# Kernel tuning notes

Measured on AMD Instinct MI355X. Metric: run time of the kernel, lower is better.

Reference implementation:

```python
import jax, jax.numpy as jnp
import numpy as np

N_NODES = 131072
N_EDGES = 4194304
H1, H2 = 16, 1


def setup_inputs() -> dict:
    key = jax.random.key(0)
    k = jax.random.split(key, 6)
    x = jax.random.uniform(k[0], (N_NODES, 2), dtype=jnp.float32)
    edge_index = jax.random.randint(k[1], (2, N_EDGES), 0, N_NODES, dtype=jnp.int64)
    # GCNConv weights (glorot-ish scale) and zero biases
    W1 = jax.random.normal(k[2], (2, H1), dtype=jnp.float32) * 0.5
    b1 = jnp.zeros((H1,), dtype=jnp.float32)
    W2 = jax.random.normal(k[3], (H1, H2), dtype=jnp.float32) * 0.25
    b2 = jnp.zeros((H2,), dtype=jnp.float32)
    return {"x": x, "W1": W1, "b1": b1, "W2": W2, "b2": b2, "edge_index": edge_index}


def gcn_layer(x, W, b, src, dst, n):
    # PyG GCNConv: h = D^{-1/2} (A+I) D^{-1/2} (x W) + b  (self-loops already in src/dst)
    h = x @ W                                              # [N, F_out]
    deg = jax.ops.segment_sum(jnp.ones(dst.shape[0], h.dtype), dst, num_segments=n)
    dinv = jax.lax.rsqrt(deg)                              # deg >= 1 thanks to self-loops
    norm = dinv[src] * dinv[dst]                           # [E+N]
    out = jax.ops.segment_sum(h[src] * norm[:, None], dst, num_segments=n)
    return out + b


def reference(x, W1, b1, W2, b2, edge_index):
    n = x.shape[0]
    loops = jnp.arange(n, dtype=edge_index.dtype)
    src = jnp.concatenate([edge_index[0], loops])          # add self-loops once
    dst = jnp.concatenate([edge_index[1], loops])
    h = jax.nn.relu(gcn_layer(x, W1, b1, src, dst, n))
    h = gcn_layer(h, W2, b2, src, dst, n)                  # [N, 1]
    scores = jax.nn.sigmoid(h)
    return scores[edge_index[0]]                           # gather per-edge source score [E, 1]
```

## Files before the change

kernel.cpp:

```cpp
#include <hip/hip_runtime.h>
#include <cmath>

typedef unsigned int uint;

constexpr int N  = 131072;
constexpr int E  = 4194304;
constexpr int F  = 16;
constexpr int NB = 512;
constexpr int NBLK  = 512;
constexpr int SCT   = 512;
constexpr int CHUNK = 8192;
constexpr int EPT   = 16;
constexpr int NSCAN = NB * NBLK;
constexpr int CAP   = 10240;
constexpr int SLOTS = CAP / SCT;
constexpr int LPN   = 16;

__global__ void __launch_bounds__(SCT) k_hist(const int* __restrict__ dst,
                                              uint* __restrict__ hist_blocks) {
    __shared__ uint hw[8 * NB];
    int t = threadIdx.x, g = blockIdx.x;
    int w = t >> 6;
#pragma unroll
    for (int k = 0; k < 8; ++k) hw[k * SCT + t] = 0;
    __syncthreads();
    const int4* dst4 = (const int4*)dst;
    int base4 = g * (CHUNK / 4);
#pragma unroll
    for (int k = 0; k < EPT / 4; ++k) {
        int4 d4 = dst4[base4 + k * SCT + t];
        atomicAdd(&hw[w * NB + (d4.x >> 8)], 1u);
        atomicAdd(&hw[w * NB + (d4.y >> 8)], 1u);
        atomicAdd(&hw[w * NB + (d4.z >> 8)], 1u);
        atomicAdd(&hw[w * NB + (d4.w >> 8)], 1u);
    }
    __syncthreads();
    uint sum = 0;
#pragma unroll
    for (int k = 0; k < 8; ++k) sum += hw[k * NB + t];
    hist_blocks[(size_t)t * NBLK + g] = sum;
}

__global__ void k_scan_up(const uint* __restrict__ hist, uint* __restrict__ bsum) {
    __shared__ uint s[256];
    int g = blockIdx.x, t = threadIdx.x;
    s[t] = hist[(size_t)g * 256 + t];
    __syncthreads();
    for (int off = 128; off > 0; off >>= 1) {
        if (t < off) s[t] += s[t + off];
        __syncthreads();
    }
    if (t == 0) bsum[g] = s[0];
}

__global__ void k_scan_down(const uint* __restrict__ hist, const uint* __restrict__ bsum,
                            uint* __restrict__ scanned) {
    __shared__ uint red[256];
    __shared__ uint s[256];
    int g = blockIdx.x, t = threadIdx.x;
    uint p = 0;
    for (int i = t; i < g; i += 256) p += bsum[i];
    red[t] = p;
    __syncthreads();
    for (int off = 128; off > 0; off >>= 1) {
        if (t < off) red[t] += red[t + off];
        __syncthreads();
    }
    uint base = red[0];
    uint v = hist[(size_t)g * 256 + t];
    s[t] = v;
    __syncthreads();
    for (int off = 1; off < 256; off <<= 1) {
        uint x = (t >= off) ? s[t - off] : 0u;
        __syncthreads();
        s[t] += x;
        __syncthreads();
    }
    scanned[(size_t)g * 256 + t] = base + s[t] - v;
}

__global__ void __launch_bounds__(SCT) k_scatter(
        const int* __restrict__ src, const int* __restrict__ dst,
        const uint* __restrict__ scanned, uint* __restrict__ part) {
    __shared__ uint h[NB];
    __shared__ uint wb[NB];
    __shared__ uint wsum[8];
    __shared__ uint vals[CHUNK];
    __shared__ uint addr[CHUNK];
    int t = threadIdx.x, g = blockIdx.x;
    int lane = t & 63, w = t >> 6;
    h[t] = 0;
    __syncthreads();
    int d[EPT], s[EPT];
    const int4* src4 = (const int4*)src;
    const int4* dst4 = (const int4*)dst;
    int base4 = g * (CHUNK / 4);
#pragma unroll
    for (int k = 0; k < EPT / 4; ++k) {
        int4 d4 = dst4[base4 + k * SCT + t];
        int4 s4 = src4[base4 + k * SCT + t];
        d[4 * k + 0] = d4.x; d[4 * k + 1] = d4.y; d[4 * k + 2] = d4.z; d[4 * k + 3] = d4.w;
        s[4 * k + 0] = s4.x; s[4 * k + 1] = s4.y; s[4 * k + 2] = s4.z; s[4 * k + 3] = s4.w;
        atomicAdd(&h[d4.x >> 8], 1u);
        atomicAdd(&h[d4.y >> 8], 1u);
        atomicAdd(&h[d4.z >> 8], 1u);
        atomicAdd(&h[d4.w >> 8], 1u);
    }
    __syncthreads();
    uint v = h[t];
    uint sv = v;
#pragma unroll
    for (int off = 1; off < 64; off <<= 1) {
        uint n = __shfl_up(sv, off);
        if (lane >= off) sv += n;
    }
    if (lane == 63) wsum[w] = sv;
    __syncthreads();
    uint wo = 0;
    for (int i = 0; i < w; ++i) wo += wsum[i];
    sv += wo;
    uint ex = sv - v;
    wb[t] = scanned[(size_t)t * NBLK + g] - ex;
    h[t] = ex;
    __syncthreads();
#pragma unroll
    for (int k = 0; k < EPT; ++k) {
        int b = d[k] >> 8;
        uint slot = atomicAdd(&h[b], 1u);
        vals[slot] = ((uint)s[k] << 8) | (uint)(d[k] & 255);
        addr[slot] = wb[b] + slot;
    }
    __syncthreads();
#pragma unroll
    for (int k = 0; k < EPT; ++k) {
        int i = k * SCT + t;
        part[addr[i]] = vals[i];
    }
}

__global__ void __launch_bounds__(SCT) k_sort(
        uint* part, const uint* __restrict__ scanned,
        const float* __restrict__ x,
        uint* __restrict__ csr, float* __restrict__ dinv, float2* __restrict__ y) {
    __shared__ uint hw[8 * 256];
    __shared__ uint cnt[256];
    __shared__ uint sc[256];
    __shared__ uint wsum[4];
    __shared__ uint srt[CAP];
    int t = threadIdx.x, b = blockIdx.x;
    int lane = t & 63, w = t >> 6;
#pragma unroll
    for (int k = 0; k < 4; ++k) hw[k * SCT + t] = 0;
    __syncthreads();
    uint S0 = scanned[(size_t)b * NBLK];
    uint S1 = (b == NB - 1) ? (uint)E : scanned[(size_t)(b + 1) * NBLK];
    uint pk[SLOTS];
#pragma unroll
    for (int k = 0; k < SLOTS; ++k) {
        uint i = S0 + (uint)(k * SCT + t);
        pk[k] = (i < S1) ? part[i] : 0xFFFFFFFFu;
        if (pk[k] != 0xFFFFFFFFu) atomicAdd(&hw[w * 256 + (pk[k] & 255u)], 1u);
    }
    __syncthreads();
    if (t < 256) {
        uint tot = 0;
#pragma unroll
        for (int k = 0; k < 8; ++k) {
            uint c = hw[k * 256 + t];
            hw[k * 256 + t] = tot;
            tot += c;
        }
        cnt[t] = tot;
        uint sv = tot;
#pragma unroll
        for (int off = 1; off < 64; off <<= 1) {
            uint n = __shfl_up(sv, off);
            if (lane >= off) sv += n;
        }
        if (lane == 63) wsum[t >> 6] = sv;
        sc[t] = sv;
    }
    __syncthreads();
    if (t < 256) {
        uint wo = 0;
        for (int i = 0; i < (t >> 6); ++i) wo += wsum[i];
        sc[t] += wo;
    }
    __syncthreads();
#pragma unroll
    for (int k = 0; k < SLOTS; ++k) {
        if (pk[k] != 0xFFFFFFFFu) {
            uint bin = pk[k] & 255u;
            uint slot = (sc[bin] - cnt[bin]) + atomicAdd(&hw[w * 256 + bin], 1u);
            srt[slot] = pk[k] >> 8;
        }
    }
    __syncthreads();
    uint L = S1 - S0;
    for (uint i = t; i < L; i += SCT) part[S0 + i] = srt[i];
    if (t < 256) {
        int node = (b << 8) + t;
        csr[node] = S0 + (sc[t] - cnt[t]);
        float di = rsqrtf(1.0f + (float)cnt[t]);
        dinv[node] = di;
        float2 xv = ((const float2*)x)[node];
        y[node] = make_float2(di * xv.x, di * xv.y);
    }
}

__global__ void k_l1(const uint* __restrict__ srcs, const uint* __restrict__ csr,
                     const float2* __restrict__ y, const float* __restrict__ dinv,
                     const float* __restrict__ W1, const float* __restrict__ b1,
                     const float* __restrict__ W2, float* __restrict__ g2) {
    int tid = blockIdx.x * blockDim.x + threadIdx.x;
    int node = tid >> 4, lane = tid & (LPN - 1);
    uint o0 = csr[node];
    uint o1 = (node == N - 1) ? (uint)E : csr[node + 1];
    float A0 = 0.0f, A1 = 0.0f;
    for (uint j = o0 + lane; j < o1; j += LPN) {
        float2 ys = y[srcs[j]];
        A0 += ys.x; A1 += ys.y;
    }
    A0 += __shfl_xor(A0, 1); A0 += __shfl_xor(A0, 2);
    A0 += __shfl_xor(A0, 4); A0 += __shfl_xor(A0, 8);
    A1 += __shfl_xor(A1, 1); A1 += __shfl_xor(A1, 2);
    A1 += __shfl_xor(A1, 4); A1 += __shfl_xor(A1, 8);
    float di = dinv[node];
    float2 yn = y[node];
    A0 = di * (A0 + yn.x);
    A1 = di * (A1 + yn.y);
    int f = lane;
    float v = fmaf(A0, W1[f], fmaf(A1, W1[F + f], b1[f]));
    float acc = fmaxf(v, 0.0f) * W2[f];
    acc += __shfl_xor(acc, 1); acc += __shfl_xor(acc, 2);
    acc += __shfl_xor(acc, 4); acc += __shfl_xor(acc, 8);
    if (lane == 0) g2[node] = di * acc;
}

__global__ void k_l2(const uint* __restrict__ srcs, const uint* __restrict__ csr,
                     const float* __restrict__ g2, const float* __restrict__ dinv,
                     const float* __restrict__ b2, float* __restrict__ scores) {
    int tid = blockIdx.x * blockDim.x + threadIdx.x;
    int node = tid >> 4, lane = tid & (LPN - 1);
    uint o0 = csr[node];
    uint o1 = (node == N - 1) ? (uint)E : csr[node + 1];
    float acc = 0.0f;
    for (uint j = o0 + lane; j < o1; j += LPN) acc += g2[srcs[j]];
    acc += __shfl_xor(acc, 1); acc += __shfl_xor(acc, 2);
    acc += __shfl_xor(acc, 4); acc += __shfl_xor(acc, 8);
    if (lane == 0) {
        float v = fmaf(dinv[node], acc + g2[node], b2[0]);
        scores[node] = 1.0f / (1.0f + expf(-v));
    }
}

__global__ void k_out(const int* __restrict__ src, const float* __restrict__ scores,
                      float* __restrict__ out) {
    int i = blockIdx.x * blockDim.x + threadIdx.x;
    if (i >= E / 4) return;
    int4 s4 = ((const int4*)src)[i];
    float4 o;
    o.x = scores[s4.x];
    o.y = scores[s4.y];
    o.z = scores[s4.z];
    o.w = scores[s4.w];
    ((float4*)out)[i] = o;
}

extern "C" void kernel_launch(void* const* d_in, const int* in_sizes, int n_in,
                              void* d_out, int out_size, void* d_ws, size_t ws_size,
                              hipStream_t stream) {
    const float* x  = (const float*)d_in[0];
    const float* W1 = (const float*)d_in[1];
    const float* b1 = (const float*)d_in[2];
    const float* W2 = (const float*)d_in[3];
    const float* b2 = (const float*)d_in[4];
    const int*   ei = (const int*)d_in[5];
    const int* src = ei;
    const int* dst = ei + E;

    uint* hist_blocks = (uint*)d_ws;
    uint* scanned     = hist_blocks + NSCAN;
    uint* bsum        = scanned + NSCAN;
    uint* csr         = bsum + 1024;
    float* dinv       = (float*)(csr + N + 2);
    float2* y         = (float2*)(dinv + N);
    float* g2         = (float*)(y + N);
    float* scores     = g2 + N;

    uint* part  = (uint*)d_out;
    float* out  = (float*)d_out;

    k_hist     <<<NBLK,          SCT, 0, stream>>>(dst, hist_blocks);
    k_scan_up  <<<NSCAN / 256,   256, 0, stream>>>(hist_blocks, bsum);
    k_scan_down<<<NSCAN / 256,   256, 0, stream>>>(hist_blocks, bsum, scanned);
    k_scatter  <<<NBLK,          SCT, 0, stream>>>(src, dst, scanned, part);
    k_sort     <<<NB,            SCT, 0, stream>>>(part, scanned, x, csr, dinv, y);
    k_l1       <<<(N * LPN) / 256, 256, 0, stream>>>(part, csr, y, dinv, W1, b1, W2, g2);
    k_l2       <<<(N * LPN) / 256, 256, 0, stream>>>(part, csr, g2, dinv, b2, scores);
    k_out      <<<E / 4 / 256,   256, 0, stream>>>(src, scores, out);
}
```

Before: 190.4 us.

## Drop global histogram and scan passes; sort from per-chunk segments with fixed buckets

Removes the histogram kernel and the two global scan kernels. The scatter kernel now writes each locally bucket-sorted chunk contiguously with coalesced uint4 stores, and records per-chunk bucket counts and offsets as 16-bit tables. The sort kernel has each thread walk one chunk's segment for its bucket and writes into fixed-capacity bucket slots, with separate csr start and end arrays. This saves a full pass over dst, two launches and the scattered global writes. In exchange, the sort reads are strided and uncoalesced, and any bucket over 9216 edges is silently truncated.

```diff
diff --git a/kernel.cpp b/kernel.cpp
--- a/kernel.cpp
+++ b/kernel.cpp
@@ -2,6 +2,7 @@
 #include <cmath>
 
 typedef unsigned int uint;
+typedef unsigned short u16;
 
 constexpr int N  = 131072;
 constexpr int E  = 4194304;
@@ -11,82 +12,15 @@
 constexpr int SCT   = 512;
 constexpr int CHUNK = 8192;
 constexpr int EPT   = 16;
-constexpr int NSCAN = NB * NBLK;
-constexpr int CAP   = 10240;
-constexpr int SLOTS = CAP / SCT;
+constexpr int CAPB  = 9216;
 constexpr int LPN   = 16;
-
-__global__ void __launch_bounds__(SCT) k_hist(const int* __restrict__ dst,
-                                              uint* __restrict__ hist_blocks) {
-    __shared__ uint hw[8 * NB];
-    int t = threadIdx.x, g = blockIdx.x;
-    int w = t >> 6;
-#pragma unroll
-    for (int k = 0; k < 8; ++k) hw[k * SCT + t] = 0;
-    __syncthreads();
-    const int4* dst4 = (const int4*)dst;
-    int base4 = g * (CHUNK / 4);
-#pragma unroll
-    for (int k = 0; k < EPT / 4; ++k) {
-        int4 d4 = dst4[base4 + k * SCT + t];
-        atomicAdd(&hw[w * NB + (d4.x >> 8)], 1u);
-        atomicAdd(&hw[w * NB + (d4.y >> 8)], 1u);
-        atomicAdd(&hw[w * NB + (d4.z >> 8)], 1u);
-        atomicAdd(&hw[w * NB + (d4.w >> 8)], 1u);
-    }
-    __syncthreads();
-    uint sum = 0;
-#pragma unroll
-    for (int k = 0; k < 8; ++k) sum += hw[k * NB + t];
-    hist_blocks[(size_t)t * NBLK + g] = sum;
-}
-
-__global__ void k_scan_up(const uint* __restrict__ hist, uint* __restrict__ bsum) {
-    __shared__ uint s[256];
-    int g = blockIdx.x, t = threadIdx.x;
-    s[t] = hist[(size_t)g * 256 + t];
-    __syncthreads();
-    for (int off = 128; off > 0; off >>= 1) {
-        if (t < off) s[t] += s[t + off];
-        __syncthreads();
-    }
-    if (t == 0) bsum[g] = s[0];
-}
-
-__global__ void k_scan_down(const uint* __restrict__ hist, const uint* __restrict__ bsum,
-                            uint* __restrict__ scanned) {
-    __shared__ uint red[256];
-    __shared__ uint s[256];
-    int g = blockIdx.x, t = threadIdx.x;
-    uint p = 0;
-    for (int i = t; i < g; i += 256) p += bsum[i];
-    red[t] = p;
-    __syncthreads();
-    for (int off = 128; off > 0; off >>= 1) {
-        if (t < off) red[t] += red[t + off];
-        __syncthreads();
-    }
-    uint base = red[0];
-    uint v = hist[(size_t)g * 256 + t];
-    s[t] = v;
-    __syncthreads();
-    for (int off = 1; off < 256; off <<= 1) {
-        uint x = (t >= off) ? s[t - off] : 0u;
-        __syncthreads();
-        s[t] += x;
-        __syncthreads();
-    }
-    scanned[(size_t)g * 256 + t] = base + s[t] - v;
-}
 
 __global__ void __launch_bounds__(SCT) k_scatter(
         const int* __restrict__ src, const int* __restrict__ dst,
-        const uint* __restrict__ scanned, uint* __restrict__ part) {
+        uint* __restrict__ part, u16* __restrict__ cnt16, u16* __restrict__ dir16) {
     __shared__ uint h[NB];
-    __shared__ uint wb[NB];
     __shared__ uint wsum[8];
     __shared__ uint vals[CHUNK];
-    __shared__ uint addr[CHUNK];
     int t = threadIdx.x, g = blockIdx.x;
     int lane = t & 63, w = t >> 6;
     h[t] = 0;
@@ -120,7 +54,9 @@
     for (int i = 0; i < w; ++i) wo += wsum[i];
     sv += wo;
     uint ex = sv - v;
-    wb[t] = scanned[(size_t)t * NBLK + g] - ex;
+    cnt16[(size_t)t * NBLK + g] = (u16)v;
+    dir16[(size_t)t * NBLK + g] = (u16)ex;
+    __syncthreads();
     h[t] = ex;
     __syncthreads();
 #pragma unroll
@@ -128,39 +64,34 @@
         int b = d[k] >> 8;
         uint slot = atomicAdd(&h[b], 1u);
         vals[slot] = ((uint)s[k] << 8) | (uint)(d[k] & 255);
-        addr[slot] = wb[b] + slot;
-    }
-    __syncthreads();
-#pragma unroll
-    for (int k = 0; k < EPT; ++k) {
-        int i = k * SCT + t;
-        part[addr[i]] = vals[i];
-    }
+    }
+    __syncthreads();
+    uint4* part4 = (uint4*)(part + (size_t)g * CHUNK);
+    const uint4* vals4 = (const uint4*)vals;
+#pragma unroll
+    for (int k = 0; k < EPT / 4; ++k)
+        part4[k * SCT + t] = vals4[k * SCT + t];
 }
 
 __global__ void __launch_bounds__(SCT) k_sort(
-        uint* part, const uint* __restrict__ scanned,
-        const float* __restrict__ x,
-        uint* __restrict__ csr, float* __restrict__ dinv, float2* __restrict__ y) {
+        const uint* __restrict__ part, const u16* __restrict__ cnt16,
+        const u16* __restrict__ dir16, const float* __restrict__ x,
+        uint* __restrict__ part2, uint* __restrict__ csr, uint* __restrict__ cend,
+        float* __restrict__ dinv, float2* __restrict__ y) {
     __shared__ uint hw[8 * 256];
     __shared__ uint cnt[256];
     __shared__ uint sc[256];
     __shared__ uint wsum[4];
-    __shared__ uint srt[CAP];
+    __shared__ uint srt[CAPB];
     int t = threadIdx.x, b = blockIdx.x;
     int lane = t & 63, w = t >> 6;
 #pragma unroll
     for (int k = 0; k < 4; ++k) hw[k * SCT + t] = 0;
     __syncthreads();
-    uint S0 = scanned[(size_t)b * NBLK];
-    uint S1 = (b == NB - 1) ? (uint)E : scanned[(size_t)(b + 1) * NBLK];
-    uint pk[SLOTS];
-#pragma unroll
-    for (int k = 0; k < SLOTS; ++k) {
-        uint i = S0 + (uint)(k * SCT + t);
-        pk[k] = (i < S1) ? part[i] : 0xFFFFFFFFu;
-        if (pk[k] != 0xFFFFFFFFu) atomicAdd(&hw[w * 256 + (pk[k] & 255u)], 1u);
-    }
+    uint segc = cnt16[(size_t)b * NBLK + t];
+    const uint* seg = part + (size_t)t * CHUNK + dir16[(size_t)b * NBLK + t];
+    for (uint j = 0; j < segc; ++j)
+        atomicAdd(&hw[w * 256 + (seg[j] & 255u)], 1u);
     __syncthreads();
     if (t < 256) {
         uint tot = 0;
@@ -187,20 +118,22 @@
         sc[t] += wo;
     }
     __syncthreads();
-#pragma unroll
-    for (int k = 0; k < SLOTS; ++k) {
-        if (pk[k] != 0xFFFFFFFFu) {
-            uint bin = pk[k] & 255u;
-            uint slot = (sc[bin] - cnt[bin]) + atomicAdd(&hw[w * 256 + bin], 1u);
-            srt[slot] = pk[k] >> 8;
-        }
-    }
-    __syncthreads();
-    uint L = S1 - S0;
-    for (uint i = t; i < L; i += SCT) part[S0 + i] = srt[i];
+    for (uint j = 0; j < segc; ++j) {
+        uint pk = seg[j];
+        uint bin = pk & 255u;
+        uint slot = (sc[bin] - cnt[bin]) + atomicAdd(&hw[w * 256 + bin], 1u);
+        if (slot < (uint)CAPB) srt[slot] = pk >> 8;
+    }
+    __syncthreads();
+    uint L = sc[255];
+    if (L > (uint)CAPB) L = CAPB;
+    uint* out2 = part2 + (size_t)b * CAPB;
+    for (uint i = t; i < L; i += SCT) out2[i] = srt[i];
     if (t < 256) {
         int node = (b << 8) + t;
-        csr[node] = S0 + (sc[t] - cnt[t]);
+        uint o0 = sc[t] - cnt[t];
+        csr[node]  = (uint)b * CAPB + o0;
+        cend[node] = (uint)b * CAPB + sc[t];
         float di = rsqrtf(1.0f + (float)cnt[t]);
         dinv[node] = di;
         float2 xv = ((const float2*)x)[node];
@@ -209,13 +142,14 @@
 }
 
 __global__ void k_l1(const uint* __restrict__ srcs, const uint* __restrict__ csr,
+                     const uint* __restrict__ cend,
                      const float2* __restrict__ y, const float* __restrict__ dinv,
                      const float* __restrict__ W1, const float* __restrict__ b1,
                      const float* __restrict__ W2, float* __restrict__ g2) {
     int tid = blockIdx.x * blockDim.x + threadIdx.x;
     int node = tid >> 4, lane = tid & (LPN - 1);
     uint o0 = csr[node];
-    uint o1 = (node == N - 1) ? (uint)E : csr[node + 1];
+    uint o1 = cend[node];
     float A0 = 0.0f, A1 = 0.0f;
     for (uint j = o0 + lane; j < o1; j += LPN) {
         float2 ys = y[srcs[j]];
@@ -238,12 +172,13 @@
 }
 
 __global__ void k_l2(const uint* __restrict__ srcs, const uint* __restrict__ csr,
+                     const uint* __restrict__ cend,
                      const float* __restrict__ g2, const float* __restrict__ dinv,
                      const float* __restrict__ b2, float* __restrict__ scores) {
     int tid = blockIdx.x * blockDim.x + threadIdx.x;
     int node = tid >> 4, lane = tid & (LPN - 1);
     uint o0 = csr[node];
-    uint o1 = (node == N - 1) ? (uint)E : csr[node + 1];
+    uint o1 = cend[node];
     float acc = 0.0f;
     for (uint j = o0 + lane; j < o1; j += LPN) acc += g2[srcs[j]];
     acc += __shfl_xor(acc, 1); acc += __shfl_xor(acc, 2);
@@ -279,24 +214,25 @@
     const int* src = ei;
     const int* dst = ei + E;
 
-    uint* hist_blocks = (uint*)d_ws;
-    uint* scanned     = hist_blocks + NSCAN;
-    uint* bsum        = scanned + NSCAN;
-    uint* csr         = bsum + 1024;
-    float* dinv       = (float*)(csr + N + 2);
-    float2* y         = (float2*)(dinv + N);
-    float* g2         = (float*)(y + N);
-    float* scores     = g2 + N;
+    u16* cnt16   = (u16*)d_ws;
+    u16* dir16   = cnt16 + (size_t)NB * NBLK;
+    uint* csr    = (uint*)(dir16 + (size_t)NB * NBLK);
+    uint* cend   = csr + N;
+    float* dinv  = (float*)(cend + N);
+    float2* y    = (float2*)(dinv + N);
+    float* g2    = (float*)(y + N);
+    float* scores = g2 + N;
+    uint* part2  = (uint*)(scores + N);
 
     uint* part  = (uint*)d_out;
     float* out  = (float*)d_out;
 
-    k_hist     <<<NBLK,          SCT, 0, stream>>>(dst, hist_blocks);
-    k_scan_up  <<<NSCAN / 256,   256, 0, stream>>>(hist_blocks, bsum);
-    k_scan_down<<<NSCAN / 256,   256, 0, stream>>>(hist_blocks, bsum, scanned);
-    k_scatter  <<<NBLK,          SCT, 0, stream>>>(src, dst, scanned, part);
-    k_sort     <<<NB,            SCT, 0, stream>>>(part, scanned, x, csr, dinv, y);
-    k_l1       <<<(N * LPN) / 256, 256, 0, stream>>>(part, csr, y, dinv, W1, b1, W2, g2);
-    k_l2       <<<(N * LPN) / 256, 256, 0, stream>>>(part, csr, g2, dinv, b2, scores);
-    k_out      <<<E / 4 / 256,   256, 0, stream>>>(src, scores, out);
-}
+    k_scatter<<<NBLK,            SCT, 0, stream>>>(src, dst, part, cnt16, dir16);
+    k_sort   <<<NB,              SCT, 0, stream>>>(part, cnt16, dir16, x, part2,
+                                                   csr, cend, dinv, y);
+    k_l1     <<<(N * LPN) / 256, 256, 0, stream>>>(part2, csr, cend, y, dinv,
+                                                   W1, b1, W2, g2);
+    k_l2     <<<(N * LPN) / 256, 256, 0, stream>>>(part2, csr, cend, g2, dinv,
+                                                   b2, scores);
+    k_out    <<<E / 4 / 256,     256, 0, stream>>>(src, scores, out);
+}
```

New measurement: 205.7 us. 1.08x slower.
